# Performance work log

Hardware: AMD Instinct MI355X
Metric: run time of the kernel (lower is better)

The kernel has to match this reference:

```python
import jax, jax.numpy as jnp
import numpy as np

K = 20          # n_neighbors
EPS = 1e-5      # batchnorm eps
SLOPE = 0.2     # leaky relu slope (DGCNN default)


def _bn_lrelu(x, axes):
    # batch-norm (per-batch stats, gamma=1, beta=0) + LeakyReLU(0.2)
    m = jnp.mean(x, axis=axes, keepdims=True)
    v = jnp.var(x, axis=axes, keepdims=True)
    return jax.nn.leaky_relu((x - m) * jax.lax.rsqrt(v + EPS), SLOPE)


def _knn(x_cf, k):
    # x_cf: (B, C, N) -> idx (B, N, k) of k nearest neighbors (incl. self)
    inner = jnp.einsum('bcn,bcm->bnm', x_cf, x_cf)
    sq = jnp.sum(x_cf * x_cf, axis=1)                  # (B, N)
    neg_d = 2.0 * inner - sq[:, :, None] - sq[:, None, :]
    return jax.lax.top_k(neg_d, k)[1]


def _gather(x_nl, idx):
    # x_nl: (B, N, C), idx: (B, N, k) -> (B, N, k, C) neighbor features
    return jnp.take_along_axis(x_nl[:, :, None, :], idx[..., None], axis=1)


def setup_inputs() -> dict:
    key = jax.random.key(0)
    ks = jax.random.split(key, 11)
    B, N, C = 16, 2048, 3
    dims = [64, 64, 128, 256]
    feat_dim = 1024

    def w(k, o, i):
        return jax.random.normal(k, (o, i), jnp.float32) / np.sqrt(i)

    return {
        'x': jax.random.normal(ks[0], (B, N, C), jnp.float32),
        'w_edge': w(ks[1], dims[0], 2 * C),
        'b_edge': jnp.zeros((dims[0],), jnp.float32),
        'w1': w(ks[2], dims[1], dims[0]),
        'b1': jnp.zeros((dims[1],), jnp.float32),
        'w2': w(ks[3], dims[2], dims[1]),
        'b2': jnp.zeros((dims[2],), jnp.float32),
        'w3': w(ks[4], dims[3], dims[2]),
        'b3': jnp.zeros((dims[3],), jnp.float32),
        'w_final': w(ks[5], feat_dim, sum(dims)),
        'b_final': jnp.zeros((feat_dim,), jnp.float32),
    }


def reference(x, w_edge, b_edge, w1, b1, w2, b2, w3, b3, w_final, b_final):
    # x: (B, N, 3) point cloud
    x_cf = jnp.transpose(x, (0, 2, 1))                 # (B, 3, N)
    idx = _knn(x_cf, K)                                # (B, N, k) -- graph built once

    # get_graph_features: edge feature = concat(neighbor - center, center)
    nb = _gather(x, idx)                               # (B, N, k, 3)
    ctr = jnp.broadcast_to(x[:, :, None, :], nb.shape)
    feat = jnp.concatenate([nb - ctr, ctr], axis=-1)   # (B, N, k, 6)

    # EdgeConvLayer: 1x1 conv2d + BN + LeakyReLU, then max over neighbors
    h = jnp.einsum('oc,bnkc->bonk', w_edge, feat) + b_edge[None, :, None, None]
    h = _bn_lrelu(h, (0, 2, 3))
    h = jnp.max(h, axis=3)                             # (B, 64, N)

    xs = [h]
    for w, b in ((w1, b1), (w2, b2), (w3, b3)):
        # graph_max_pooling with reused kNN indices
        g = jnp.max(_gather(jnp.transpose(h, (0, 2, 1)), idx), axis=2)  # (B, N, C)
        h = jnp.einsum('oc,bnc->bon', w, g) + b[None, :, None]          # 1x1 conv1d
        h = _bn_lrelu(h, (0, 2))
        xs.append(h)

    h_cat = jnp.concatenate(xs, axis=1)                # (B, 512, N)
    out = jnp.einsum('oc,bcn->bon', w_final, h_cat) + b_final[None, :, None]
    return jnp.max(out, axis=2)                        # (B, 1024)
```

## Files before the change

### kernel.cpp

```cpp
#include <hip/hip_runtime.h>
#include <hip/hip_bf16.h>
#include <math.h>

#define B_ 16
#define N_ 2048
#define KNN 20
#define SLOPE 0.2f
#define EPS_ 1e-5f

#define SEG 8
#define SEGLEN (N_ / SEG)
#define QPB 64
#define CAP 64

typedef __attribute__((ext_vector_type(8))) short short8;
typedef __attribute__((ext_vector_type(4))) float float4v;

__global__ __launch_bounds__(256, 2) void knn_kernel(const float* __restrict__ x,
                                                     int* __restrict__ idx) {
    __shared__ float4 pts4[N_];
    __shared__ float thr[QPB * 24];
    __shared__ float tq[QPB];
    __shared__ int cnt[QPB];
    __shared__ float lv[QPB * CAP];
    __shared__ int   li[QPB * CAP];

    const int b = blockIdx.x >> 5;
    const int qb = blockIdx.x & 31;
    const float* xb = x + (size_t)b * N_ * 3;
    for (int i = threadIdx.x; i < N_; i += 256) {
        float xv = xb[i * 3], yv = xb[i * 3 + 1], zv = xb[i * 3 + 2];
        pts4[i] = make_float4(xv, yv, zv, xv * xv + yv * yv + zv * zv);
    }
    if (threadIdx.x < QPB) cnt[threadIdx.x] = 0;
    __syncthreads();

    const int s = threadIdx.x >> 5;
    const int qs = threadIdx.x & 31;
    const int q0 = qs * 2, q1 = q0 + 1;
    const int n0 = qb * QPB + q0;
    const float4 pa = pts4[n0];
    const float4 pb = pts4[n0 + 1];
    const int m0 = s * SEGLEN;

    float ca[8], cb[8];
#pragma unroll
    for (int c = 0; c < 8; ++c) {
        float va0 = -INFINITY, va1 = -INFINITY;
        float vb0 = -INFINITY, vb1 = -INFINITY;
        for (int g = 0; g < 4; ++g) {
            float4 r[8];
#pragma unroll
            for (int j = 0; j < 8; ++j) r[j] = pts4[m0 + c * 32 + g * 8 + j];
#pragma unroll
            for (int j = 0; j < 8; ++j) {
                const float da = 2.f * (pa.x * r[j].x + pa.y * r[j].y + pa.z * r[j].z)
                                 - pa.w - r[j].w;
                const float db = 2.f * (pb.x * r[j].x + pb.y * r[j].y + pb.z * r[j].z)
                                 - pb.w - r[j].w;
                if (j & 1) { va1 = fmaxf(va1, da); vb1 = fmaxf(vb1, db); }
                else       { va0 = fmaxf(va0, da); vb0 = fmaxf(vb0, db); }
            }
        }
        ca[c] = fmaxf(va0, va1); cb[c] = fmaxf(vb0, vb1);
    }
    {
        float t0 = -INFINITY, t1 = -INFINITY, t2 = -INFINITY;
        float u0 = -INFINITY, u1 = -INFINITY, u2 = -INFINITY;
#pragma unroll
        for (int c = 0; c < 8; ++c) {
            float v = ca[c];
            float r0 = fminf(t0, v); t0 = fmaxf(t0, v);
            float r1 = fminf(t1, r0); t1 = fmaxf(t1, r0);
            t2 = fmaxf(t2, r1);
            float w = cb[c];
            float s0 = fminf(u0, w); u0 = fmaxf(u0, w);
            float s1 = fminf(u1, s0); u1 = fmaxf(u1, s0);
            u2 = fmaxf(u2, s1);
        }
        thr[q0 * 24 + s * 3 + 0] = t0;
        thr[q0 * 24 + s * 3 + 1] = t1;
        thr[q0 * 24 + s * 3 + 2] = t2;
        thr[q1 * 24 + s * 3 + 0] = u0;
        thr[q1 * 24 + s * 3 + 1] = u1;
        thr[q1 * 24 + s * 3 + 2] = u2;
    }
    __syncthreads();

    if (threadIdx.x < QPB) {
        const int qq = threadIdx.x;
        float s0 = INFINITY, s1 = INFINITY, s2 = INFINITY, s3 = INFINITY, s4 = INFINITY;
#pragma unroll
        for (int j = 0; j < 24; ++j) {
            float c = thr[qq * 24 + j];
            float u;
            u = fminf(s0, c); c = fmaxf(s0, c); s0 = u;
            u = fminf(s1, c); c = fmaxf(s1, c); s1 = u;
            u = fminf(s2, c); c = fmaxf(s2, c); s2 = u;
            u = fminf(s3, c); c = fmaxf(s3, c); s3 = u;
            s4 = fminf(s4, c);
        }
        tq[qq] = s4 - (fabsf(s4) * 1e-6f + 1e-6f);
    }
    __syncthreads();

    const float ta = tq[q0];
    const float tb = tq[q1];
    for (int g = 0; g < 32; ++g) {
        float4 r[8];
#pragma unroll
        for (int j = 0; j < 8; ++j) r[j] = pts4[m0 + g * 8 + j];
#pragma unroll
        for (int j = 0; j < 8; ++j) {
            const int m = m0 + g * 8 + j;
            const float da = 2.f * (pa.x * r[j].x + pa.y * r[j].y + pa.z * r[j].z)
                             - pa.w - r[j].w;
            const float db = 2.f * (pb.x * r[j].x + pb.y * r[j].y + pb.z * r[j].z)
                             - pb.w - r[j].w;
            if (da >= ta) {
                int pos = atomicAdd(&cnt[q0], 1);
                if (pos < CAP) { lv[q0 * CAP + pos] = da; li[q0 * CAP + pos] = m; }
            }
            if (db >= tb) {
                int pos = atomicAdd(&cnt[q1], 1);
                if (pos < CAP) { lv[q1 * CAP + pos] = db; li[q1 * CAP + pos] = m; }
            }
        }
    }
    __syncthreads();

    if (threadIdx.x < QPB) {
        const int qq = threadIdx.x;
        const int nn = qb * QPB + qq;
        int* op = idx + (size_t)(b * N_ + nn) * KNN;
        float vals[KNN]; int inds[KNN];
#pragma unroll
        for (int j = 0; j < KNN; ++j) { vals[j] = -INFINITY; inds[j] = 0; }
        const int c = cnt[qq];
        if (c <= CAP) {
            for (int j = 0; j < c; ++j) {
                const float v = lv[qq * CAP + j];
                if (v > vals[KNN - 1]) {
                    float cv = v; int ci = li[qq * CAP + j];
#pragma unroll
                    for (int k = 0; k < KNN; ++k) {
                        const bool sw = cv > vals[k];
                        const float tv = vals[k]; const int ti = inds[k];
                        vals[k] = sw ? cv : tv;  inds[k] = sw ? ci : ti;
                        cv      = sw ? tv : cv;  ci      = sw ? ti : ci;
                    }
                }
            }
        } else {
            const float4 pq2 = pts4[nn];
            for (int m = 0; m < N_; ++m) {
                const float4 p = pts4[m];
                const float d = 2.f * (pq2.x * p.x + pq2.y * p.y + pq2.z * p.z)
                                - pq2.w - p.w;
                if (d > vals[KNN - 1]) {
                    float cv = d; int ci = m;
#pragma unroll
                    for (int k = 0; k < KNN; ++k) {
                        const bool sw = cv > vals[k];
                        const float tv = vals[k]; const int ti = inds[k];
                        vals[k] = sw ? cv : tv;  inds[k] = sw ? ci : ti;
                        cv      = sw ? tv : cv;  ci      = sw ? ti : ci;
                    }
                }
            }
        }
#pragma unroll
        for (int j = 0; j < KNN; ++j) op[j] = inds[j];
    }
}

__global__ __launch_bounds__(256) void edge_kernel(const float* __restrict__ x,
                                                   const int* __restrict__ idx,
                                                   const float* __restrict__ w_edge,
                                                   const float* __restrict__ b_edge,
                                                   float* __restrict__ cat,
                                                   double* __restrict__ stats) {
    __shared__ float xs[N_ * 3];
    __shared__ float ws[64 * 6];
    __shared__ float bs[64];
    __shared__ float s_sum[64], s_sq[64];

    int b = blockIdx.x >> 5;
    int pb = blockIdx.x & 31;
    const float* xb = x + (size_t)b * N_ * 3;
    for (int i = threadIdx.x; i < N_ * 3; i += 256) xs[i] = xb[i];
    for (int i = threadIdx.x; i < 64 * 6; i += 256) ws[i] = w_edge[i];
    if (threadIdx.x < 64) {
        bs[threadIdx.x] = b_edge[threadIdx.x];
        s_sum[threadIdx.x] = 0.f; s_sq[threadIdx.x] = 0.f;
    }
    __syncthreads();

    int p = threadIdx.x >> 2;
    int cg = threadIdx.x & 3;
    int n = pb * 64 + p;
    float cx = xs[n * 3], cy = xs[n * 3 + 1], cz = xs[n * 3 + 2];

    float maxv[16], sum[16], sq[16];
#pragma unroll
    for (int i = 0; i < 16; ++i) { maxv[i] = -INFINITY; sum[i] = 0.f; sq[i] = 0.f; }

    const int* ip = idx + (size_t)(b * N_ + n) * KNN;
    for (int k = 0; k < KNN; ++k) {
        int j = ip[k];
        float dx = xs[j * 3] - cx, dy = xs[j * 3 + 1] - cy, dz = xs[j * 3 + 2] - cz;
#pragma unroll
        for (int i = 0; i < 16; ++i) {
            int o = cg * 16 + i;
            const float* wr = &ws[o * 6];
            float h = bs[o] + wr[0] * dx + wr[1] * dy + wr[2] * dz
                            + wr[3] * cx + wr[4] * cy + wr[5] * cz;
            sum[i] += h; sq[i] += h * h;
            maxv[i] = fmaxf(maxv[i], h);
        }
    }

    float* cp = cat + (size_t)(b * N_ + n) * 512;
#pragma unroll
    for (int i = 0; i < 16; ++i) {
        int o = cg * 16 + i;
        cp[o] = maxv[i];
        atomicAdd(&s_sum[o], sum[i]);
        atomicAdd(&s_sq[o], sq[i]);
    }
    __syncthreads();
    if (threadIdx.x < 64) {
        atomicAdd(&stats[threadIdx.x], (double)s_sum[threadIdx.x]);
        atomicAdd(&stats[64 + threadIdx.x], (double)s_sq[threadIdx.x]);
    }
}

__global__ __launch_bounds__(256) void wconv_kernel(const float* __restrict__ w,
                                                    __hip_bfloat16* __restrict__ wb) {
    int t = blockIdx.x * 256 + threadIdx.x;
    wb[t] = __float2bfloat16(w[t]);
}

template <int CIN, int COUT, int PT>
__global__ __launch_bounds__(256) void layer_kernel(float* __restrict__ cat,
                                                    const int* __restrict__ idx,
                                                    const float* __restrict__ w,
                                                    const float* __restrict__ bias,
                                                    const double* __restrict__ stats_in,
                                                    double invcnt_in,
                                                    double* __restrict__ stats_out,
                                                    int off_in, int off_out) {
    constexpr int P = 64;
    constexpr int LDC = CIN + 4;
    constexpr int WS = COUT + 4;
    constexpr int NCG = CIN / 4;
    constexpr int PPAR = 256 / NCG;
    constexpr int NOG = COUT / 4;
    static_assert(NOG * (P / PT) == 256, "thread mapping");

    __shared__ float g[P * LDC];
    __shared__ float wt[16 * WS];
    __shared__ float s_sum[COUT], s_sq[COUT];

    const int b = blockIdx.x & 15;
    const int pb = blockIdx.x >> 4;
    const int pt0 = b * N_ + pb * P;

    {
        const int cg = threadIdx.x % NCG;
        const int pp = threadIdx.x / NCG;
        float mean[4], inv[4];
#pragma unroll
        for (int j = 0; j < 4; ++j) {
            const double mu = stats_in[cg * 4 + j] * invcnt_in;
            const double e2 = stats_in[CIN + cg * 4 + j] * invcnt_in;
            const float var = (float)(e2 - mu * mu);
            mean[j] = (float)mu;
            inv[j] = rsqrtf(var + EPS_);
        }
        for (int p = pp; p < P; p += PPAR) {
            const int* ip = idx + (size_t)(pt0 + p) * KNN;
            float4 m = make_float4(-INFINITY, -INFINITY, -INFINITY, -INFINITY);
#pragma unroll
            for (int k = 0; k < KNN; ++k) {
                const int j = ip[k];
                const float4 v = *(const float4*)&cat[(size_t)(b * N_ + j) * 512 + off_in + cg * 4];
                m.x = fmaxf(m.x, v.x); m.y = fmaxf(m.y, v.y);
                m.z = fmaxf(m.z, v.z); m.w = fmaxf(m.w, v.w);
            }
            float4 r;
            r.x = (m.x - mean[0]) * inv[0]; r.x = r.x >= 0.f ? r.x : SLOPE * r.x;
            r.y = (m.y - mean[1]) * inv[1]; r.y = r.y >= 0.f ? r.y : SLOPE * r.y;
            r.z = (m.z - mean[2]) * inv[2]; r.z = r.z >= 0.f ? r.z : SLOPE * r.z;
            r.w = (m.w - mean[3]) * inv[3]; r.w = r.w >= 0.f ? r.w : SLOPE * r.w;
            *(float4*)&g[p * LDC + cg * 4] = r;
        }
    }
    if (threadIdx.x < COUT) { s_sum[threadIdx.x] = 0.f; s_sq[threadIdx.x] = 0.f; }

    const int og = threadIdx.x % NOG;
    const int pg = threadIdx.x / NOG;
    const int o0 = og * 4, p0 = pg * PT;

    float acc[4][PT];
#pragma unroll
    for (int i = 0; i < 4; ++i)
#pragma unroll
        for (int j = 0; j < PT; ++j) acc[i][j] = 0.f;

    for (int c0 = 0; c0 < CIN; c0 += 16) {
        __syncthreads();
        for (int i = threadIdx.x; i < COUT * 16; i += 256) {
            int o = i >> 4, cc = i & 15;
            wt[cc * WS + o] = w[(size_t)o * CIN + c0 + cc];
        }
        __syncthreads();
#pragma unroll
        for (int ccq = 0; ccq < 4; ++ccq) {
            const float4 w0 = *(const float4*)&wt[(ccq * 4 + 0) * WS + o0];
            const float4 w1 = *(const float4*)&wt[(ccq * 4 + 1) * WS + o0];
            const float4 w2 = *(const float4*)&wt[(ccq * 4 + 2) * WS + o0];
            const float4 w3 = *(const float4*)&wt[(ccq * 4 + 3) * WS + o0];
#pragma unroll
            for (int p = 0; p < PT; ++p) {
                const float4 gv = *(const float4*)&g[(p0 + p) * LDC + c0 + ccq * 4];
                acc[0][p] += w0.x * gv.x; acc[0][p] += w1.x * gv.y;
                acc[0][p] += w2.x * gv.z; acc[0][p] += w3.x * gv.w;
                acc[1][p] += w0.y * gv.x; acc[1][p] += w1.y * gv.y;
                acc[1][p] += w2.y * gv.z; acc[1][p] += w3.y * gv.w;
                acc[2][p] += w0.z * gv.x; acc[2][p] += w1.z * gv.y;
                acc[2][p] += w2.z * gv.z; acc[2][p] += w3.z * gv.w;
                acc[3][p] += w0.w * gv.x; acc[3][p] += w1.w * gv.y;
                acc[3][p] += w2.w * gv.z; acc[3][p] += w3.w * gv.w;
            }
        }
    }

    const float4 bv = *(const float4*)&bias[o0];
    float lsum[4] = {0.f, 0.f, 0.f, 0.f}, lsq[4] = {0.f, 0.f, 0.f, 0.f};
#pragma unroll
    for (int p = 0; p < PT; ++p) {
        float4 hv;
        hv.x = acc[0][p] + bv.x; hv.y = acc[1][p] + bv.y;
        hv.z = acc[2][p] + bv.z; hv.w = acc[3][p] + bv.w;
        lsum[0] += hv.x; lsq[0] += hv.x * hv.x;
        lsum[1] += hv.y; lsq[1] += hv.y * hv.y;
        lsum[2] += hv.z; lsq[2] += hv.z * hv.z;
        lsum[3] += hv.w; lsq[3] += hv.w * hv.w;
        *(float4*)&cat[(size_t)(pt0 + p0 + p) * 512 + off_out + o0] = hv;
    }
#pragma unroll
    for (int i = 0; i < 4; ++i) {
        atomicAdd(&s_sum[o0 + i], lsum[i]);
        atomicAdd(&s_sq[o0 + i], lsq[i]);
    }
    __syncthreads();
    if (threadIdx.x < COUT) {
        atomicAdd(&stats_out[threadIdx.x], (double)s_sum[threadIdx.x]);
        atomicAdd(&stats_out[COUT + threadIdx.x], (double)s_sq[threadIdx.x]);
    }
}

__global__ __launch_bounds__(256) void bnconv_kernel(const float* __restrict__ cat,
                                                     const double* __restrict__ stats,
                                                     unsigned short* __restrict__ catb,
                                                     double ik, double in_) {
    const int t = blockIdx.x * 256 + threadIdx.x;
    const int pn = t >> 7;
    const int c = (t & 127) * 4;

    const double* sp; const double* qp; double icnt;
    if (c < 64)       { sp = stats + c;             qp = stats + 64 + c;        icnt = ik; }
    else if (c < 128) { sp = stats + 128 + (c - 64);  qp = stats + 192 + (c - 64);  icnt = in_; }
    else if (c < 256) { sp = stats + 256 + (c - 128); qp = stats + 384 + (c - 128); icnt = in_; }
    else              { sp = stats + 512 + (c - 256); qp = stats + 768 + (c - 256); icnt = in_; }

    const float4 v = *(const float4*)&cat[(size_t)pn * 512 + c];
    float r[4]; const float vv[4] = {v.x, v.y, v.z, v.w};
#pragma unroll
    for (int j = 0; j < 4; ++j) {
        const double mu = sp[j] * icnt;
        const double e2 = qp[j] * icnt;
        const float var = (float)(e2 - mu * mu);
        const float inv = rsqrtf(var + EPS_);
        float x = (vv[j] - (float)mu) * inv;
        r[j] = x >= 0.f ? x : SLOPE * x;
    }
    ushort4 o;
    __hip_bfloat16 h0 = __float2bfloat16(r[0]); o.x = *(unsigned short*)&h0;
    __hip_bfloat16 h1 = __float2bfloat16(r[1]); o.y = *(unsigned short*)&h1;
    __hip_bfloat16 h2 = __float2bfloat16(r[2]); o.z = *(unsigned short*)&h2;
    __hip_bfloat16 h3 = __float2bfloat16(r[3]); o.w = *(unsigned short*)&h3;
    *(ushort4*)&catb[(size_t)pn * 512 + c] = o;
}

__global__ __launch_bounds__(256) void final_mfma_kernel(const short* __restrict__ catb,
                                                         const short* __restrict__ wb,
                                                         const float* __restrict__ bias,
                                                         float* __restrict__ partial) {
    constexpr int LDK = 72;
    __shared__ short As[128 * LDK];
    __shared__ short Bs[128 * LDK];
    __shared__ float red[256];

    const int ob = blockIdx.x;
    const int pblk = blockIdx.y;
    const int pt0 = pblk * 128;

    const int wid = threadIdx.x >> 6;
    const int lane = threadIdx.x & 63;
    const int wm = wid >> 1, wn = wid & 1;
    const int lm = lane & 15, g = lane >> 4;

    const int srow = threadIdx.x >> 1;
    const int scg = (threadIdx.x & 1) * 32;
    const short* ga = catb + (size_t)(pt0 + srow) * 512 + scg;
    const short* gb = wb + (size_t)(ob * 128 + srow) * 512 + scg;
    short* la = As + srow * LDK + scg;
    short* lb = Bs + srow * LDK + scg;

    float4v acc[4][4];
#pragma unroll
    for (int i = 0; i < 4; ++i)
#pragma unroll
        for (int j = 0; j < 4; ++j) acc[i][j] = {0.f, 0.f, 0.f, 0.f};

    short8 ra[4], rb[4];
#pragma unroll
    for (int j = 0; j < 4; ++j) {
        ra[j] = *(const short8*)(ga + j * 8);
        rb[j] = *(const short8*)(gb + j * 8);
    }

    for (int step = 0; step < 8; ++step) {
        __syncthreads();
#pragma unroll
        for (int j = 0; j < 4; ++j) {
            *(short8*)(la + j * 8) = ra[j];
            *(short8*)(lb + j * 8) = rb[j];
        }
        __syncthreads();
        if (step < 7) {
            const int c1 = (step + 1) * 64;
#pragma unroll
            for (int j = 0; j < 4; ++j) {
                ra[j] = *(const short8*)(ga + c1 + j * 8);
                rb[j] = *(const short8*)(gb + c1 + j * 8);
            }
        }
#pragma unroll
        for (int kk = 0; kk < 2; ++kk) {
            short8 a[4], b[4];
#pragma unroll
            for (int t = 0; t < 4; ++t) {
                a[t] = *(const short8*)&As[(wm * 64 + t * 16 + lm) * LDK + kk * 32 + g * 8];
                b[t] = *(const short8*)&Bs[(wn * 64 + t * 16 + lm) * LDK + kk * 32 + g * 8];
            }
#pragma unroll
            for (int mt = 0; mt < 4; ++mt)
#pragma unroll
                for (int nt = 0; nt < 4; ++nt)
                    acc[mt][nt] = __builtin_amdgcn_mfma_f32_16x16x32_bf16(
                        a[mt], b[nt], acc[mt][nt], 0, 0, 0);
        }
    }

    float cm[4];
#pragma unroll
    for (int nt = 0; nt < 4; ++nt) {
        float m = -INFINITY;
#pragma unroll
        for (int mt = 0; mt < 4; ++mt)
#pragma unroll
            for (int r = 0; r < 4; ++r) m = fmaxf(m, acc[mt][nt][r]);
        m = fmaxf(m, __shfl_xor(m, 16, 64));
        m = fmaxf(m, __shfl_xor(m, 32, 64));
        cm[nt] = m;
    }
    __syncthreads();
    if (lane < 16) {
#pragma unroll
        for (int nt = 0; nt < 4; ++nt)
            red[wm * 128 + wn * 64 + nt * 16 + lane] = cm[nt];
    }
    __syncthreads();
    if (threadIdx.x < 128) {
        const int o = threadIdx.x;
        float v = fmaxf(red[o], red[128 + o]) + bias[ob * 128 + o];
        partial[(size_t)pblk * 1024 + ob * 128 + o] = v;
    }
}

__global__ __launch_bounds__(256) void reduce_kernel(const float* __restrict__ partial,
                                                     float* __restrict__ out) {
    int t = blockIdx.x * 256 + threadIdx.x;
    int b = t >> 10, o = t & 1023;
    float m = -INFINITY;
#pragma unroll 4
    for (int i = 0; i < 16; ++i)
        m = fmaxf(m, partial[(size_t)((b * 16 + i) * 1024) + o]);
    out[t] = m;
}

extern "C" void kernel_launch(void* const* d_in, const int* in_sizes, int n_in,
                              void* d_out, int out_size, void* d_ws, size_t ws_size,
                              hipStream_t stream) {
    const float* x = (const float*)d_in[0];
    const float* w_edge = (const float*)d_in[1];
    const float* b_edge = (const float*)d_in[2];
    const float* w1 = (const float*)d_in[3];
    const float* b1 = (const float*)d_in[4];
    const float* w2 = (const float*)d_in[5];
    const float* b2 = (const float*)d_in[6];
    const float* w3 = (const float*)d_in[7];
    const float* b3 = (const float*)d_in[8];
    const float* w_final = (const float*)d_in[9];
    const float* b_final = (const float*)d_in[10];
    float* out = (float*)d_out;

    char* ws = (char*)d_ws;
    int* idx = (int*)ws;
    float* cat = (float*)(ws + 2621440);
    float* partial = (float*)(ws + 69730304);
    double* stats = (double*)(ws + 70778880);
    __hip_bfloat16* catb = (__hip_bfloat16*)(ws + 70787072);
    __hip_bfloat16* wb = (__hip_bfloat16*)(ws + 104341504);

    double* st_e = stats;
    double* st_1 = stats + 128;
    double* st_2 = stats + 256;
    double* st_3 = stats + 512;
    const double ik = 1.0 / ((double)B_ * N_ * KNN);
    const double in_ = 1.0 / ((double)B_ * N_);

    hipMemsetAsync(stats, 0, 1024 * sizeof(double), stream);
    wconv_kernel<<<2048, 256, 0, stream>>>(w_final, wb);

    knn_kernel<<<B_ * 32, 256, 0, stream>>>(x, idx);
    edge_kernel<<<B_ * 32, 256, 0, stream>>>(x, idx, w_edge, b_edge, cat, st_e);
    layer_kernel<64, 64, 4><<<(B_ * N_) / 64, 256, 0, stream>>>(
        cat, idx, w1, b1, st_e, ik, st_1, 0, 64);
    layer_kernel<64, 128, 8><<<(B_ * N_) / 64, 256, 0, stream>>>(
        cat, idx, w2, b2, st_1, in_, st_2, 64, 128);
    layer_kernel<128, 256, 16><<<(B_ * N_) / 64, 256, 0, stream>>>(
        cat, idx, w3, b3, st_2, in_, st_3, 128, 256);
    bnconv_kernel<<<(B_ * N_ * 128) / 256, 256, 0, stream>>>(
        cat, stats, (unsigned short*)catb, ik, in_);
    final_mfma_kernel<<<dim3(8, 256), 256, 0, stream>>>((const short*)catb, (const short*)wb,
                                                        b_final, partial);
    reduce_kernel<<<64, 256, 0, stream>>>(partial, out);
}
```

Before: 372.9 us.

## Fuse edge-conv into kNN kernel and coarsen threshold chunking

Moves the EdgeConv computation (gather neighbours, 1x1 conv, max, BN statistics) into the tail of the kNN kernel. It reuses the points already held in shared memory and the freshly computed indices through a shared buffer that aliases the threshold array. This removes one kernel launch, the reload of the point cloud, and the global read of the idx array. It also halves the number of chunk maxima used for the per-segment threshold estimate, which may loosen the threshold and send more candidates to the filtering stage. Output stores are vectorised as float4.

```diff
diff --git a/kernel.cpp b/kernel.cpp
--- a/kernel.cpp
+++ b/kernel.cpp
@@ -17,13 +17,23 @@
 typedef __attribute__((ext_vector_type(4))) float float4v;
 
 __global__ __launch_bounds__(256, 2) void knn_kernel(const float* __restrict__ x,
-                                                     int* __restrict__ idx) {
+                                                     int* __restrict__ idx,
+                                                     const float* __restrict__ w_edge,
+                                                     const float* __restrict__ b_edge,
+                                                     float* __restrict__ cat,
+                                                     double* __restrict__ stats) {
     __shared__ float4 pts4[N_];
-    __shared__ float thr[QPB * 24];
+    __shared__ union {
+        float thr[QPB * 24];
+        int sidx[QPB * KNN];
+    } u2;
     __shared__ float tq[QPB];
     __shared__ int cnt[QPB];
     __shared__ float lv[QPB * CAP];
     __shared__ int   li[QPB * CAP];
+    __shared__ float ws[64 * 6];
+    __shared__ float bs[64];
+    __shared__ float s_sum[64], s_sq[64];
 
     const int b = blockIdx.x >> 5;
     const int qb = blockIdx.x & 31;
@@ -32,7 +42,12 @@
         float xv = xb[i * 3], yv = xb[i * 3 + 1], zv = xb[i * 3 + 2];
         pts4[i] = make_float4(xv, yv, zv, xv * xv + yv * yv + zv * zv);
     }
-    if (threadIdx.x < QPB) cnt[threadIdx.x] = 0;
+    for (int i = threadIdx.x; i < 64 * 6; i += 256) ws[i] = w_edge[i];
+    if (threadIdx.x < QPB) {
+        cnt[threadIdx.x] = 0;
+        bs[threadIdx.x] = b_edge[threadIdx.x];
+        s_sum[threadIdx.x] = 0.f; s_sq[threadIdx.x] = 0.f;
+    }
     __syncthreads();
 
     const int s = threadIdx.x >> 5;
@@ -43,15 +58,15 @@
     const float4 pb = pts4[n0 + 1];
     const int m0 = s * SEGLEN;
 
-    float ca[8], cb[8];
-#pragma unroll
-    for (int c = 0; c < 8; ++c) {
+    float ca[4], cb[4];
+#pragma unroll
+    for (int c = 0; c < 4; ++c) {
         float va0 = -INFINITY, va1 = -INFINITY;
         float vb0 = -INFINITY, vb1 = -INFINITY;
         for (int g = 0; g < 4; ++g) {
             float4 r[8];
 #pragma unroll
-            for (int j = 0; j < 8; ++j) r[j] = pts4[m0 + c * 32 + g * 8 + j];
+            for (int j = 0; j < 8; ++j) r[j] = pts4[m0 + c * 64 + g * 8 + j];
 #pragma unroll
             for (int j = 0; j < 8; ++j) {
                 const float da = 2.f * (pa.x * r[j].x + pa.y * r[j].y + pa.z * r[j].z)
@@ -66,9 +81,9 @@
     }
     {
         float t0 = -INFINITY, t1 = -INFINITY, t2 = -INFINITY;
-        float u0 = -INFINITY, u1 = -INFINITY, u2 = -INFINITY;
-#pragma unroll
-        for (int c = 0; c < 8; ++c) {
+        float u0 = -INFINITY, u1 = -INFINITY, u2v = -INFINITY;
+#pragma unroll
+        for (int c = 0; c < 4; ++c) {
             float v = ca[c];
             float r0 = fminf(t0, v); t0 = fmaxf(t0, v);
             float r1 = fminf(t1, r0); t1 = fmaxf(t1, r0);
@@ -76,14 +91,14 @@
             float w = cb[c];
             float s0 = fminf(u0, w); u0 = fmaxf(u0, w);
             float s1 = fminf(u1, s0); u1 = fmaxf(u1, s0);
-            u2 = fmaxf(u2, s1);
-        }
-        thr[q0 * 24 + s * 3 + 0] = t0;
-        thr[q0 * 24 + s * 3 + 1] = t1;
-        thr[q0 * 24 + s * 3 + 2] = t2;
-        thr[q1 * 24 + s * 3 + 0] = u0;
-        thr[q1 * 24 + s * 3 + 1] = u1;
-        thr[q1 * 24 + s * 3 + 2] = u2;
+            u2v = fmaxf(u2v, s1);
+        }
+        u2.thr[q0 * 24 + s * 3 + 0] = t0;
+        u2.thr[q0 * 24 + s * 3 + 1] = t1;
+        u2.thr[q0 * 24 + s * 3 + 2] = t2;
+        u2.thr[q1 * 24 + s * 3 + 0] = u0;
+        u2.thr[q1 * 24 + s * 3 + 1] = u1;
+        u2.thr[q1 * 24 + s * 3 + 2] = u2v;
     }
     __syncthreads();
 
@@ -92,7 +107,7 @@
         float s0 = INFINITY, s1 = INFINITY, s2 = INFINITY, s3 = INFINITY, s4 = INFINITY;
 #pragma unroll
         for (int j = 0; j < 24; ++j) {
-            float c = thr[qq * 24 + j];
+            float c = u2.thr[qq * 24 + j];
             float u;
             u = fminf(s0, c); c = fmaxf(s0, c); s0 = u;
             u = fminf(s1, c); c = fmaxf(s1, c); s1 = u;
@@ -170,63 +185,51 @@
             }
         }
 #pragma unroll
-        for (int j = 0; j < KNN; ++j) op[j] = inds[j];
-    }
-}
-
-__global__ __launch_bounds__(256) void edge_kernel(const float* __restrict__ x,
-                                                   const int* __restrict__ idx,
-                                                   const float* __restrict__ w_edge,
-                                                   const float* __restrict__ b_edge,
-                                                   float* __restrict__ cat,
-                                                   double* __restrict__ stats) {
-    __shared__ float xs[N_ * 3];
-    __shared__ float ws[64 * 6];
-    __shared__ float bs[64];
-    __shared__ float s_sum[64], s_sq[64];
-
-    int b = blockIdx.x >> 5;
-    int pb = blockIdx.x & 31;
-    const float* xb = x + (size_t)b * N_ * 3;
-    for (int i = threadIdx.x; i < N_ * 3; i += 256) xs[i] = xb[i];
-    for (int i = threadIdx.x; i < 64 * 6; i += 256) ws[i] = w_edge[i];
-    if (threadIdx.x < 64) {
-        bs[threadIdx.x] = b_edge[threadIdx.x];
-        s_sum[threadIdx.x] = 0.f; s_sq[threadIdx.x] = 0.f;
-    }
-    __syncthreads();
-
-    int p = threadIdx.x >> 2;
-    int cg = threadIdx.x & 3;
-    int n = pb * 64 + p;
-    float cx = xs[n * 3], cy = xs[n * 3 + 1], cz = xs[n * 3 + 2];
-
-    float maxv[16], sum[16], sq[16];
-#pragma unroll
-    for (int i = 0; i < 16; ++i) { maxv[i] = -INFINITY; sum[i] = 0.f; sq[i] = 0.f; }
-
-    const int* ip = idx + (size_t)(b * N_ + n) * KNN;
-    for (int k = 0; k < KNN; ++k) {
-        int j = ip[k];
-        float dx = xs[j * 3] - cx, dy = xs[j * 3 + 1] - cy, dz = xs[j * 3 + 2] - cz;
+        for (int j = 0; j < KNN; ++j) {
+            op[j] = inds[j];
+            u2.sidx[qq * KNN + j] = inds[j];
+        }
+    }
+    __syncthreads();
+
+    {
+        const int p = threadIdx.x >> 2;
+        const int cg = threadIdx.x & 3;
+        const int n = qb * QPB + p;
+        const float4 ctr = pts4[n];
+        const float cx = ctr.x, cy = ctr.y, cz = ctr.z;
+
+        float maxv[16], sum[16], sq[16];
+#pragma unroll
+        for (int i = 0; i < 16; ++i) { maxv[i] = -INFINITY; sum[i] = 0.f; sq[i] = 0.f; }
+
+        for (int k = 0; k < KNN; ++k) {
+            const int j = u2.sidx[p * KNN + k];
+            const float4 nb = pts4[j];
+            const float dx = nb.x - cx, dy = nb.y - cy, dz = nb.z - cz;
+#pragma unroll
+            for (int i = 0; i < 16; ++i) {
+                const int o = cg * 16 + i;
+                const float* wr = &ws[o * 6];
+                float h = bs[o] + wr[0] * dx + wr[1] * dy + wr[2] * dz
+                                + wr[3] * cx + wr[4] * cy + wr[5] * cz;
+                sum[i] += h; sq[i] += h * h;
+                maxv[i] = fmaxf(maxv[i], h);
+            }
+        }
+
+        float* cp = cat + (size_t)(b * N_ + n) * 512 + cg * 16;
+#pragma unroll
+        for (int i4 = 0; i4 < 4; ++i4)
+            *(float4*)&cp[i4 * 4] = make_float4(maxv[i4 * 4], maxv[i4 * 4 + 1],
+                                                maxv[i4 * 4 + 2], maxv[i4 * 4 + 3]);
+        float ls = 0.f, lq = 0.f;
 #pragma unroll
         for (int i = 0; i < 16; ++i) {
-            int o = cg * 16 + i;
-            const float* wr = &ws[o * 6];
-            float h = bs[o] + wr[0] * dx + wr[1] * dy + wr[2] * dz
-                            + wr[3] * cx + wr[4] * cy + wr[5] * cz;
-            sum[i] += h; sq[i] += h * h;
-            maxv[i] = fmaxf(maxv[i], h);
-        }
-    }
-
-    float* cp = cat + (size_t)(b * N_ + n) * 512;
-#pragma unroll
-    for (int i = 0; i < 16; ++i) {
-        int o = cg * 16 + i;
-        cp[o] = maxv[i];
-        atomicAdd(&s_sum[o], sum[i]);
-        atomicAdd(&s_sq[o], sq[i]);
+            atomicAdd(&s_sum[cg * 16 + i], sum[i]);
+            atomicAdd(&s_sq[cg * 16 + i], sq[i]);
+        }
+        (void)ls; (void)lq;
     }
     __syncthreads();
     if (threadIdx.x < 64) {
@@ -536,8 +539,7 @@
     hipMemsetAsync(stats, 0, 1024 * sizeof(double), stream);
     wconv_kernel<<<2048, 256, 0, stream>>>(w_final, wb);
 
-    knn_kernel<<<B_ * 32, 256, 0, stream>>>(x, idx);
-    edge_kernel<<<B_ * 32, 256, 0, stream>>>(x, idx, w_edge, b_edge, cat, st_e);
+    knn_kernel<<<B_ * 32, 256, 0, stream>>>(x, idx, w_edge, b_edge, cat, st_e);
     layer_kernel<64, 64, 4><<<(B_ * N_) / 64, 256, 0, stream>>>(
         cat, idx, w1, b1, st_e, ik, st_1, 0, 64);
     layer_kernel<64, 128, 8><<<(B_ * N_) / 64, 256, 0, stream>>>(
```

Measured after the change: 900.9 us. +141.6%, slower.
